# Optimization experiments

Hardware: AMD Instinct MI355X
Metric: run time of the kernel (lower is better)

## Reference

```python
import jax, jax.numpy as jnp
import numpy as np

DIM = 512
HEADS = 4
HEAD_DIM = DIM // HEADS
SCALE = HEAD_DIM ** -0.5


def _lin(x, W, b):
    # torch nn.Linear: y = x @ W.T + b, W is [out, in]
    return jnp.einsum('...i,oi->...o', x, W) + b


def setup_inputs() -> dict:
    key = jax.random.key(0)
    ks = jax.random.split(key, 20)
    f1 = jax.random.normal(ks[0], (4, 5, DIM, 10, 10), dtype=jnp.float32)
    f2 = jax.random.normal(ks[1], (4, 75, DIM, 10, 10), dtype=jnp.float32)
    names = ['k1', 'v1', 'q2', 'k2', 'v2', 'o1', 'o2']
    inp = {'f1': f1, 'f2': f2}
    for i, nm in enumerate(names):
        inp['W' + nm] = 0.02 * jax.random.normal(ks[2 + 2 * i], (DIM, DIM), dtype=jnp.float32)
        inp['b' + nm] = 0.02 * jax.random.normal(ks[3 + 2 * i], (DIM,), dtype=jnp.float32)
    return inp


def _forward(f1, f2, Wk1, bk1, Wv1, bv1, Wq2, bq2, Wk2, bk2, Wv2, bv2, Wo1, bo1, Wo2, bo2):
    B, n1, C, H, W = f1.shape
    n2 = f2.shape[1]
    L = H * W
    # [B,n,C,H,W] -> [B,n,L,C]
    f1t = f1.reshape(B, n1, C, L).transpose(0, 1, 3, 2)
    f2t = f2.reshape(B, n2, C, L).transpose(0, 1, 3, 2)

    def split_heads(x, n):  # [B,n,L,C] -> [B,heads,n*L,hd]
        return x.reshape(B, n * L, HEADS, HEAD_DIM).transpose(0, 2, 1, 3)

    def merge_heads(x, n):  # [B,heads,n*L,hd] -> [B,n,L,C]
        return x.transpose(0, 2, 1, 3).reshape(B, n, L, C)

    K1 = split_heads(_lin(f1t, Wk1, bk1), n1)
    V1 = split_heads(_lin(f1t, Wv1, bv1), n1)
    Q2 = split_heads(_lin(f2t, Wq2, bq2), n2)
    K2 = split_heads(_lin(f2t, Wk2, bk2), n2)  # computed as in original, unused downstream
    V2 = split_heads(_lin(f2t, Wv2, bv2), n2)

    # Query attends to support: [B,h,n2*L,n1*L]
    att_q = jax.nn.softmax(jnp.einsum('bhqd,bhkd->bhqk', Q2, K1) * SCALE, axis=-1)
    out2 = jnp.einsum('bhqk,bhkd->bhqd', att_q, V1)
    out2 = _lin(merge_heads(out2, n2), Wo2, bo2)
    out2 = out2.transpose(0, 1, 3, 2).reshape(B, n2, C, H, W)

    # Support attends to query: [B,h,n1*L,n2*L]
    att_s = jax.nn.softmax(jnp.einsum('bhsd,bhqd->bhsq', K1, Q2) * SCALE, axis=-1)
    out1 = jnp.einsum('bhsq,bhqd->bhsd', att_s, V2)
    out1 = _lin(merge_heads(out1, n1), Wo1, bo1)
    out1 = out1.transpose(0, 1, 3, 2).reshape(B, n1, C, H, W)
    return (out1, out2)


def reference(f1, f2, Wk1, bk1, Wv1, bv1, Wq2, bq2, Wk2, bk2, Wv2, bv2, Wo1, bo1, Wo2, bo2):
    return _forward(f1, f2, Wk1, bk1, Wv1, bv1, Wq2, bq2, Wk2, bk2, Wv2, bv2, Wo1, bo1, Wo2, bo2)
```

## Files before the change

kernel.cpp:

```cpp
#include <hip/hip_runtime.h>
#include <hip/hip_bf16.h>


#define QSCL  (0.08838834764831845f * 1.4426950408889634f)
#define KSPL  8
#define NRB2  59
#define NRB1  4

using bf16x8 = __attribute__((ext_vector_type(8))) short;
using f32x4  = __attribute__((ext_vector_type(4))) float;

__device__ inline ushort f2bf(float x) {
    union { float f; unsigned u; } v; v.f = x;
    unsigned r = v.u + 0x7fff + ((v.u >> 16) & 1);
    return (ushort)(r >> 16);
}

__device__ inline void gll16(const ushort* g, ushort* l) {
    __builtin_amdgcn_global_load_lds(
        (const __attribute__((address_space(1))) void*)g,
        (__attribute__((address_space(3))) void*)l, 16, 0, 0);
}

struct PreArgs { const float* w[6]; float s[6]; const float* f1; const float* f2; };

__global__ __launch_bounds__(256) void pre_kernel(
    PreArgs pa, ushort* __restrict__ Wb,
    ushort* __restrict__ f1t, ushort* __restrict__ f2t)
{
    __shared__ ushort Ts[100 * 136];
    const int t   = threadIdx.x;
    const int bid = blockIdx.x;

    if (bid < 1536) {
        const int wsel = bid >> 8;
        const float* src = pa.w[wsel];
        const float sc = pa.s[wsel];
        ushort* d = Wb + (size_t)wsel * 262144;
        const int idx = ((bid & 255) * 256 + t) * 4;
        const float4 v = *(const float4*)(src + idx);
        ushort4 o;
        o.x = f2bf(v.x * sc); o.y = f2bf(v.y * sc);
        o.z = f2bf(v.z * sc); o.w = f2bf(v.w * sc);
        *(ushort4*)(d + idx) = o;
        return;
    }

    const int bn = bid - 1536;
    const float* Xb;
    ushort* Yb;
    if (bn < 20) { Xb = pa.f1 + (size_t)bn * 51200;        Yb = f1t + (size_t)bn * 51200; }
    else         { Xb = pa.f2 + (size_t)(bn - 20) * 51200; Yb = f2t + (size_t)(bn - 20) * 51200; }

    for (int c0 = 0; c0 < 512; c0 += 128) {
        __syncthreads();
        #pragma unroll
        for (int i = 0; i < 50; ++i) {
            const int id = i * 256 + t;
            const int c = id / 100, l = id - c * 100;
            Ts[l * 136 + c] = f2bf(Xb[(size_t)(c0 + c) * 100 + l]);
        }
        __syncthreads();
        #pragma unroll
        for (int i = 0; i < 7; ++i) {
            const int id = i * 256 + t;
            if (id < 1600) {
                const int cg = id & 15, l = id >> 4;
                *(uint4*)(Yb + (size_t)l * 512 + c0 + cg * 8) =
                    *(const uint4*)&Ts[l * 136 + cg * 8];
            }
        }
    }
}

struct GemmJob {
    const ushort* A; const ushort* B;
    const float* bias; void* C;
    size_t sA, sB, sC;
    float bscale;
    int ldC, Mrows, Ncols, gx, gy, nblk;
};

template<int EPI, int BAXIS>
__global__ __launch_bounds__(256) void gemm_nt(GemmJob j0, GemmJob j1)
{
    __shared__ ushort smem[17408];
    ushort* As = smem;
    ushort* Bs = smem + 8192;

    const bool second = (int)blockIdx.x >= j0.nblk;
    const GemmJob& j = second ? j1 : j0;
    int id = blockIdx.x - (second ? j0.nblk : 0);

    const int bx = id % j.gx;
    const int rem = id / j.gx;
    const int by = rem % j.gy;
    const int bz = rem / j.gy;

    const int t    = threadIdx.x;
    const int lane = t & 63;
    const int w    = t >> 6;
    const int mw   = (w >> 1) * 64;
    const int nw   = (w & 1) * 64;
    const int m0   = bx * 128;
    const int n0   = by * 128;
    const int Mrows = j.Mrows, Ncols = j.Ncols, ldC = j.ldC;
    const ushort* Ab = j.A + (size_t)bz * j.sA;
    const ushort* Bb = j.B + (size_t)bz * j.sB;
    const float* bias = j.bias;

    f32x4 acc[4][4];
    #pragma unroll
    for (int i = 0; i < 4; ++i)
        #pragma unroll
        for (int jj = 0; jj < 4; ++jj) acc[i][jj] = (f32x4){0.f, 0.f, 0.f, 0.f};

    const int lr = lane >> 3;
    const int cb = lane & 7;

    for (int k0 = 0; k0 < 512; k0 += 64) {
        if (k0) __syncthreads();
        #pragma unroll
        for (int i = 0; i < 4; ++i) {
            const int row = w * 32 + i * 8 + lr;
            const int ar = min(m0 + row, Mrows - 1);
            gll16(Ab + (size_t)ar * 512 + k0 + ((cb ^ (row & 7)) * 8),
                  As + (w * 32 + i * 8) * 64);
            const int br = min(n0 + row, Ncols - 1);
            gll16(Bb + (size_t)br * 512 + k0 + ((cb ^ (row & 7)) * 8),
                  Bs + (w * 32 + i * 8) * 64);
        }
        __syncthreads();
        #pragma unroll
        for (int ks = 0; ks < 2; ++ks) {
            bf16x8 af[4], bv[4];
            #pragma unroll
            for (int mf = 0; mf < 4; ++mf) {
                const int row = mw + mf * 16 + (lane & 15);
                af[mf] = *(const bf16x8*)((const char*)As + row * 128 +
                          ((ks * 64 + (lane >> 4) * 16) ^ ((row & 7) << 4)));
            }
            #pragma unroll
            for (int nf = 0; nf < 4; ++nf) {
                const int row = nw + nf * 16 + (lane & 15);
                bv[nf] = *(const bf16x8*)((const char*)Bs + row * 128 +
                          ((ks * 64 + (lane >> 4) * 16) ^ ((row & 7) << 4)));
            }
            #pragma unroll
            for (int mf = 0; mf < 4; ++mf)
                #pragma unroll
                for (int nf = 0; nf < 4; ++nf)
                    acc[mf][nf] = __builtin_amdgcn_mfma_f32_16x16x32_bf16(
                        af[mf], bv[nf], acc[mf][nf], 0, 0, 0);
        }
    }
    __syncthreads();

    if (EPI == 0) {
        float bcol[4];
        if (BAXIS == 1) {
            #pragma unroll
            for (int nf = 0; nf < 4; ++nf)
                bcol[nf] = bias[n0 + nw + nf * 16 + (lane & 15)] * j.bscale;
        }
        ushort* Ts = smem;
        #pragma unroll
        for (int mf = 0; mf < 4; ++mf) {
            #pragma unroll
            for (int r = 0; r < 4; ++r) {
                const int row = mw + mf * 16 + (lane >> 4) * 4 + r;
                const float brow = (BAXIS == 0) ? bias[m0 + row] * j.bscale : 0.f;
                #pragma unroll
                for (int nf = 0; nf < 4; ++nf) {
                    const int col = nw + nf * 16 + (lane & 15);
                    const float v = acc[mf][nf][r] +
                                    ((BAXIS == 1) ? bcol[nf] : brow);
                    Ts[row * 136 + col] = f2bf(v);
                }
            }
        }
        __syncthreads();
        ushort* Cb = (ushort*)j.C + (size_t)bz * j.sC;
        #pragma unroll
        for (int i = 0; i < 8; ++i) {
            const int id2 = i * 256 + t;
            const int row = id2 >> 4, cg = id2 & 15;
            if (m0 + row < Mrows)
                *(uint4*)(Cb + (size_t)(m0 + row) * ldC + n0 + cg * 8) =
                    *(const uint4*)&Ts[row * 136 + cg * 8];
        }
    } else {
        float* Ts2 = (float*)smem;
        float* Cb = (float*)j.C + (size_t)bz * j.sC;
        const int colL = t & 127;
        const int rb2 = t >> 7;
        const int tg = n0 + colL;
        int nIdx = 0, lIdx = 0;
        if (tg < Ncols) { nIdx = tg / 100; lIdx = tg - nIdx * 100; }
        #pragma unroll
        for (int h = 0; h < 2; ++h) {
            __syncthreads();
            if ((mw >> 6) == h) {
                #pragma unroll
                for (int mf = 0; mf < 4; ++mf) {
                    #pragma unroll
                    for (int r = 0; r < 4; ++r) {
                        const int rowl = mf * 16 + (lane >> 4) * 4 + r;
                        const float brow = bias[m0 + h * 64 + rowl];
                        #pragma unroll
                        for (int nf = 0; nf < 4; ++nf) {
                            const int col = nw + nf * 16 + (lane & 15);
                            Ts2[rowl * 132 + col] = acc[mf][nf][r] + brow;
                        }
                    }
                }
            }
            __syncthreads();
            if (tg < Ncols) {
                float* dst = Cb + (size_t)nIdx * 51200 + lIdx;
                #pragma unroll
                for (int i = 0; i < 32; ++i) {
                    const int rowl = i * 2 + rb2;
                    const int c = m0 + h * 64 + rowl;
                    dst[(size_t)c * 100] = Ts2[rowl * 132 + colL];
                }
            }
        }
    }
}

__global__ __launch_bounds__(512, 4) void attn_mfma_kernel(
    const ushort* __restrict__ Q2, const ushort* __restrict__ K1,
    const ushort* __restrict__ V1t, const ushort* __restrict__ V2t,
    ushort* __restrict__ A2, float* __restrict__ PartO, float* __restrict__ Pml)
{
    __shared__ ushort Ks[64 * 128];
    __shared__ ushort Vs[128 * 64];

    const int t    = threadIdx.x;
    const int lane = t & 63;
    const int w    = t >> 6;

    const int flat = blockIdx.x;
    const int xcd = flat & 7, ii = flat >> 3;
    const bool dir2 = (ii >= 64);
    int rb, h, b, sp = 0;
    if (dir2) {
        const int w2 = xcd * 118 + (ii - 64);
        rb = w2 % NRB2;
        const int hb = w2 / NRB2;
        h = hb & 3; b = hb >> 2;
    } else {
        const int w1 = xcd * 64 + ii;
        rb = w1 & 3; sp = (w1 >> 2) & 7;
        const int hb = w1 >> 5;
        h = hb & 3; b = hb >> 2;
    }

    const int TR = dir2 ? 7500 : 500;
    const int TK = dir2 ? 500 : 7500;
    const int strideV = dir2 ? 512 : 7552;
    const ushort* R  = dir2 ? Q2 : K1;
    const ushort* Kt = dir2 ? K1 : Q2;
    const ushort* Vt = dir2 ? V1t : V2t;

    const int r0 = rb * 128;
    const int ho = h * 128;

    int kbeg = 0, kend = TK;
    if (!dir2) {
        kbeg = sp * 938;
        kend = kbeg + 938; if (kend > TK) kend = TK;
    }

    bf16x8 qa[4];
    {
        const ushort* Rb = R + (size_t)b * TR * 512;
        const int qrow = min(r0 + (w << 4) + (lane & 15), TR - 1);
        const ushort* qp = Rb + (size_t)qrow * 512 + ho + (lane >> 4) * 8;
        #pragma unroll
        for (int s = 0; s < 4; ++s)
            qa[s] = *(const bf16x8*)(qp + s * 32);
    }

    const ushort* Kb = Kt + (size_t)b * TK * 512;
    const ushort* Vb = Vt + ((size_t)b * 512 + ho) * strideV;

    const int krow_i = lane >> 4;
    const int kcol   = (lane & 15) * 8;
    const int vrow_i = lane >> 3;
    const int vcol   = (lane & 7) * 8;
    const int gq     = lane >> 4;

    float m_run = -3.0e38f, l_run = 0.f;
    f32x4 acc[8];
    #pragma unroll
    for (int g = 0; g < 8; ++g) acc[g] = (f32x4){0.f, 0.f, 0.f, 0.f};

    #pragma unroll
    for (int i = 0; i < 2; ++i) {
        const int kr = w * 8 + i * 4 + krow_i;
        gll16(Kb + (size_t)(kbeg + kr) * 512 + ho + (kcol ^ ((kr & 7) << 3)),
              Ks + (w * 8 + i * 4) * 128);
    }

    for (int kbase = kbeg; kbase < kend; kbase += 64) {
        #pragma unroll
        for (int i = 0; i < 2; ++i) {
            const int vd = w * 16 + i * 8 + vrow_i;
            gll16(Vb + (size_t)vd * strideV + kbase + (vcol ^ ((vd & 7) << 3)),
                  Vs + (w * 16 + i * 8) * 64);
        }
        asm volatile("s_waitcnt vmcnt(2)" ::: "memory");
        __builtin_amdgcn_s_barrier();
        __builtin_amdgcn_sched_barrier(0);

        f32x4 sf[4];
        __builtin_amdgcn_s_setprio(1);
        #pragma unroll
        for (int f = 0; f < 4; ++f) {
            f32x4 s = (f32x4){0.f, 0.f, 0.f, 0.f};
            const int kr = f * 16 + (lane & 15);
            const int kb2 = kr * 256, sw = (kr & 7) << 4, g16 = gq * 16;
            #pragma unroll
            for (int s4 = 0; s4 < 4; ++s4) {
                bf16x8 kf = *(const bf16x8*)((const char*)Ks + kb2 + ((s4 * 64 + g16) ^ sw));
                s = __builtin_amdgcn_mfma_f32_16x16x32_bf16(kf, qa[s4], s, 0, 0, 0);
            }
            sf[f] = s;
        }
        __builtin_amdgcn_s_setprio(0);

        if (kbase + 64 > kend) {
            #pragma unroll
            for (int f = 0; f < 4; ++f)
                #pragma unroll
                for (int r = 0; r < 4; ++r)
                    if (kbase + f * 16 + gq * 4 + r >= kend) sf[f][r] = -3.0e38f;
        }
        float mx = sf[0][0];
        #pragma unroll
        for (int f = 0; f < 4; ++f)
            #pragma unroll
            for (int r = 0; r < 4; ++r) mx = fmaxf(mx, sf[f][r]);
        mx = fmaxf(mx, __shfl_xor(mx, 16));
        mx = fmaxf(mx, __shfl_xor(mx, 32));
        if (__any(mx > m_run + 11.0f)) {
            const float mn = fmaxf(m_run, mx);
            const float sc = __builtin_amdgcn_exp2f(m_run - mn);
            m_run = mn;
            l_run *= sc;
            float scal4[4];
            #pragma unroll
            for (int r = 0; r < 4; ++r)
                scal4[r] = __shfl(sc, (lane & 48) + gq * 4 + r);
            #pragma unroll
            for (int g = 0; g < 8; ++g)
                #pragma unroll
                for (int r = 0; r < 4; ++r) acc[g][r] *= scal4[r];
        }
        float rs = 0.f;
        #pragma unroll
        for (int f = 0; f < 4; ++f)
            #pragma unroll
            for (int r = 0; r < 4; ++r) {
                const float p = __builtin_amdgcn_exp2f(sf[f][r] - m_run);
                sf[f][r] = p;
                rs += p;
            }
        rs += __shfl_xor(rs, 16);
        rs += __shfl_xor(rs, 32);
        l_run += rs;

        uint pk[4][2];
        #pragma unroll
        for (int f = 0; f < 4; ++f) {
            const float x0 = sf[f][0], x1 = sf[f][1], x2 = sf[f][2], x3 = sf[f][3];
            asm("v_cvt_pk_bf16_f32 %0, %1, %2" : "=v"(pk[f][0]) : "v"(x0), "v"(x1));
            asm("v_cvt_pk_bf16_f32 %0, %1, %2" : "=v"(pk[f][1]) : "v"(x2), "v"(x3));
        }
        union { uint u[4]; bf16x8 v; } pa0, pa1;
        #pragma unroll
        for (int u = 0; u < 4; ++u) {
            const int srcl = (lane & 15) + ((lane & 16) << 1) + ((u >> 1) << 4);
            const uint a0 = (uint)__shfl((int)pk[0][u & 1], srcl);
            const uint b0 = (uint)__shfl((int)pk[1][u & 1], srcl);
            const uint a1 = (uint)__shfl((int)pk[2][u & 1], srcl);
            const uint b1 = (uint)__shfl((int)pk[3][u & 1], srcl);
            pa0.u[u] = (lane & 32) ? b0 : a0;
            pa1.u[u] = (lane & 32) ? b1 : a1;
        }

        asm volatile("s_waitcnt vmcnt(0)" ::: "memory");
        __builtin_amdgcn_s_barrier();
        __builtin_amdgcn_sched_barrier(0);

        if (kbase + 64 < kend) {
            #pragma unroll
            for (int i = 0; i < 2; ++i) {
                const int kr = w * 8 + i * 4 + krow_i;
                gll16(Kb + (size_t)(kbase + 64 + kr) * 512 + ho + (kcol ^ ((kr & 7) << 3)),
                      Ks + (w * 8 + i * 4) * 128);
            }
        }

        {
            const int g16 = gq * 16;
            __builtin_amdgcn_s_setprio(1);
            #pragma unroll
            for (int g = 0; g < 8; ++g) {
                const int dr = g * 16 + (lane & 15);
                const int vb = dr * 128, vsw = (dr & 7) << 4;
                bf16x8 v0 = *(const bf16x8*)((const char*)Vs + vb + ((g16) ^ vsw));
                bf16x8 v1 = *(const bf16x8*)((const char*)Vs + vb + ((64 + g16) ^ vsw));
                acc[g] = __builtin_amdgcn_mfma_f32_16x16x32_bf16(pa0.v, v0, acc[g], 0, 0, 0);
                acc[g] = __builtin_amdgcn_mfma_f32_16x16x32_bf16(pa1.v, v1, acc[g], 0, 0, 0);
            }
            __builtin_amdgcn_s_setprio(0);
        }
        __builtin_amdgcn_s_barrier();
        __builtin_amdgcn_sched_barrier(0);
    }

    const int rloc = (w << 4) + (gq << 2);
    if (dir2) {
        float linv[4];
        #pragma unroll
        for (int r = 0; r < 4; ++r)
            linv[r] = 1.f / __shfl(l_run, (lane & 48) + gq * 4 + r);
        #pragma unroll
        for (int r = 0; r < 4; ++r) {
            const int row = r0 + rloc + r;
            if (row < TR) {
                ushort* Ab2 = A2 + ((size_t)b * TR + row) * 512 + ho + (lane & 15);
                #pragma unroll
                for (int g = 0; g < 8; ++g) Ab2[g * 16] = f2bf(acc[g][r] * linv[r]);
            }
        }
    } else {
        const size_t tile = (((size_t)b * 4 + h) * NRB1 + rb) * KSPL + sp;
        float* Po = PartO + tile * (128 * 128);
        float* Pm = Pml + tile * 256;
        #pragma unroll
        for (int r = 0; r < 4; ++r) {
            const int row = rloc + r;
            float* pp = Po + row * 128 + (lane & 15);
            #pragma unroll
            for (int g = 0; g < 8; ++g) pp[g * 16] = acc[g][r];
        }
        if (lane < 16) {
            Pm[(w << 4) + lane] = m_run;
            Pm[128 + (w << 4) + lane] = l_run;
        }
    }
}

__global__ __launch_bounds__(256) void attn_combine_kernel(
    const float* __restrict__ PartO, const float* __restrict__ Pml,
    ushort* __restrict__ Aout, int TR)
{
    const int t = threadIdx.x;
    const int rb = blockIdx.x >> 1, half = blockIdx.x & 1;
    const int h = blockIdx.y, b = blockIdx.z;
    const int row = half * 64 + (t >> 2);
    const int dq = (t & 3) * 32;
    const int r0 = rb * 128;
    const size_t tbase = (((size_t)b * 4 + h) * NRB1 + rb) * KSPL;

    float M = -3.0e38f;
    #pragma unroll
    for (int i = 0; i < KSPL; ++i)
        M = fmaxf(M, Pml[(tbase + i) * 256 + row]);
    float wt[KSPL], L = 0.f;
    #pragma unroll
    for (int i = 0; i < KSPL; ++i) {
        const float wi = __builtin_amdgcn_exp2f(Pml[(tbase + i) * 256 + row] - M);
        wt[i] = wi;
        L += wi * Pml[(tbase + i) * 256 + 128 + row];
    }
    if (r0 + row >= TR) return;
    const float invL = 1.f / L;

    float o[32];
    #pragma unroll
    for (int j = 0; j < 32; ++j) o[j] = 0.f;
    #pragma unroll
    for (int i = 0; i < KSPL; ++i) {
        const float* pp = PartO + (tbase + i) * (128 * 128) + row * 128 + dq;
        #pragma unroll
        for (int j = 0; j < 32; j += 4) {
            const float4 v = *(const float4*)(pp + j);
            o[j] += wt[i] * v.x; o[j+1] += wt[i] * v.y;
            o[j+2] += wt[i] * v.z; o[j+3] += wt[i] * v.w;
        }
    }
    ushort* Ab = Aout + ((size_t)b * TR + r0 + row) * 512 + h * 128 + dq;
    #pragma unroll
    for (int j = 0; j < 32; j += 4) {
        ushort4 v;
        v.x = f2bf(o[j] * invL); v.y = f2bf(o[j+1] * invL);
        v.z = f2bf(o[j+2] * invL); v.w = f2bf(o[j+3] * invL);
        *(ushort4*)(Ab + j) = v;
    }
}

extern "C" void kernel_launch(void* const* d_in, const int* in_sizes, int n_in,
                              void* d_out, int out_size, void* d_ws, size_t ws_size,
                              hipStream_t stream) {
    const float* f1  = (const float*)d_in[0];
    const float* f2  = (const float*)d_in[1];
    const float* Wk1 = (const float*)d_in[2];
    const float* bk1 = (const float*)d_in[3];
    const float* Wv1 = (const float*)d_in[4];
    const float* bv1 = (const float*)d_in[5];
    const float* Wq2 = (const float*)d_in[6];
    const float* bq2 = (const float*)d_in[7];
    const float* Wv2 = (const float*)d_in[10];
    const float* bv2 = (const float*)d_in[11];
    const float* Wo1 = (const float*)d_in[12];
    const float* bo1 = (const float*)d_in[13];
    const float* Wo2 = (const float*)d_in[14];
    const float* bo2 = (const float*)d_in[15];
    float* out = (float*)d_out;

    ushort* f1t = (ushort*)d_ws;
    ushort* f2t = f1t + (size_t)1024000;
    ushort* Wb  = f2t + (size_t)15360000;
    ushort* K1  = Wb  + (size_t)1572864;
    ushort* Q2  = K1  + (size_t)1024000;
    ushort* V1t = Q2  + (size_t)15360000;
    ushort* V2t = V1t + (size_t)1048576;
    ushort* A1  = V2t + (size_t)15466496;
    ushort* A2  = A1  + (size_t)1024000;
    float* PartO = (float*)(A2 + (size_t)15360000);
    float* Pml   = PartO + (size_t)512*128*128;

    const dim3 blk(256);

    const ushort* Wk1b = Wb;
    const ushort* Wv1b = Wb + 262144;
    const ushort* Wq2b = Wb + 2*262144;
    const ushort* Wv2b = Wb + 3*262144;
    const ushort* Wo1b = Wb + 4*262144;
    const ushort* Wo2b = Wb + 5*262144;

    PreArgs pa;
    pa.w[0]=Wk1; pa.w[1]=Wv1; pa.w[2]=Wq2; pa.w[3]=Wv2; pa.w[4]=Wo1; pa.w[5]=Wo2;
    pa.s[0]=1.f; pa.s[1]=1.f; pa.s[2]=QSCL; pa.s[3]=1.f; pa.s[4]=1.f; pa.s[5]=1.f;
    pa.f1 = f1; pa.f2 = f2;
    pre_kernel<<<dim3(1856), blk, 0, stream>>>(pa, Wb, f1t, f2t);

    GemmJob jK{f1t, Wk1b, bk1, K1, 0, 0, 0, 1.f, 512, 2000, 512, 16, 4, 64};
    GemmJob jQ{f2t, Wq2b, bq2, Q2, 0, 0, 0, QSCL, 512, 30000, 512, 235, 4, 940};
    gemm_nt<0,1><<<dim3(1004), blk, 0, stream>>>(jK, jQ);

    GemmJob jV1{Wv1b, f1t, bv1, V1t, 0, (size_t)500*512, (size_t)512*512, 1.f,
                512, 512, 500, 4, 4, 64};
    GemmJob jV2{Wv2b, f2t, bv2, V2t, 0, (size_t)7500*512, (size_t)512*7552, 1.f,
                7552, 512, 7500, 4, 59, 944};
    gemm_nt<0,0><<<dim3(1008), blk, 0, stream>>>(jV1, jV2);

    attn_mfma_kernel<<<dim3(1456), dim3(512), 0, stream>>>(
        Q2, K1, V1t, V2t, A2, PartO, Pml);
    attn_combine_kernel<<<dim3(8, 4, 4), blk, 0, stream>>>(PartO, Pml, A1, 500);

    GemmJob jO1{Wo1b, A1, bo1, out, 0, (size_t)500*512, (size_t)5*51200, 1.f,
                0, 512, 500, 4, 4, 64};
    GemmJob jO2{Wo2b, A2, bo2, out + (size_t)1024000, 0, (size_t)7500*512,
                (size_t)75*51200, 1.f, 0, 512, 7500, 4, 59, 944};
    gemm_nt<2,0><<<dim3(1008), blk, 0, stream>>>(jO1, jO2);
}
```

Baseline: 258.6 us.

## Merge QK and V projection GEMMs into one launch with XCD-aware block remap

The K1/Q2 projection and V1/V2 projection GEMM launches are fused into a single launch covering four jobs. Block ids are remapped so that each of the 8 XCDs gets a contiguous range of work, and the K/Q jobs iterate the N dimension fastest, so neighbouring tiles that share A rows land on the same XCD's L2. This aims to remove one launch gap and tail, and to improve L2 reuse. The bias axis becomes a runtime field, which adds per-thread branching in the epilogue.

```diff
diff --git a/kernel.cpp b/kernel.cpp
--- a/kernel.cpp
+++ b/kernel.cpp
@@ -78,32 +78,47 @@
     const float* bias; void* C;
     size_t sA, sB, sC;
     float bscale;
-    int ldC, Mrows, Ncols, gx, gy, nblk;
+    int ldC, Mrows, Ncols, gx, gy, fastn, baxis, nblk;
 };
 
-template<int EPI, int BAXIS>
-__global__ __launch_bounds__(256) void gemm_nt(GemmJob j0, GemmJob j1)
+struct GemmJobs { GemmJob j0, j1, j2, j3; int ntot; };
+
+template<int EPI>
+__global__ __launch_bounds__(256) void gemm_nt(GemmJobs J)
 {
     __shared__ ushort smem[17408];
     ushort* As = smem;
     ushort* Bs = smem + 8192;
 
-    const bool second = (int)blockIdx.x >= j0.nblk;
-    const GemmJob& j = second ? j1 : j0;
-    int id = blockIdx.x - (second ? j0.nblk : 0);
-
-    const int bx = id % j.gx;
+    const int ntot = J.ntot;
+    const int q8 = ntot >> 3, r8 = ntot & 7;
+    const int xcd = blockIdx.x & 7, ii = blockIdx.x >> 3;
+    const int work = (xcd < r8 ? xcd * (q8 + 1)
+                               : r8 * (q8 + 1) + (xcd - r8) * q8) + ii;
+
+    GemmJob j; int id;
+    {
+        const int c0 = J.j0.nblk;
+        const int c1 = c0 + J.j1.nblk;
+        const int c2 = c1 + J.j2.nblk;
+        if (work < c0)      { j = J.j0; id = work; }
+        else if (work < c1) { j = J.j1; id = work - c0; }
+        else if (work < c2) { j = J.j2; id = work - c1; }
+        else                { j = J.j3; id = work - c2; }
+    }
+
+    const int fx = id % j.gx;
     const int rem = id / j.gx;
-    const int by = rem % j.gy;
+    const int fy = rem % j.gy;
     const int bz = rem / j.gy;
+    const int m0 = (j.fastn ? fy : fx) * 128;
+    const int n0 = (j.fastn ? fx : fy) * 128;
 
     const int t    = threadIdx.x;
     const int lane = t & 63;
     const int w    = t >> 6;
     const int mw   = (w >> 1) * 64;
     const int nw   = (w & 1) * 64;
-    const int m0   = bx * 128;
-    const int n0   = by * 128;
     const int Mrows = j.Mrows, Ncols = j.Ncols, ldC = j.ldC;
     const ushort* Ab = j.A + (size_t)bz * j.sA;
     const ushort* Bb = j.B + (size_t)bz * j.sB;
@@ -158,7 +173,7 @@
 
     if (EPI == 0) {
         float bcol[4];
-        if (BAXIS == 1) {
+        if (j.baxis == 1) {
             #pragma unroll
             for (int nf = 0; nf < 4; ++nf)
                 bcol[nf] = bias[n0 + nw + nf * 16 + (lane & 15)] * j.bscale;
@@ -169,12 +184,12 @@
             #pragma unroll
             for (int r = 0; r < 4; ++r) {
                 const int row = mw + mf * 16 + (lane >> 4) * 4 + r;
-                const float brow = (BAXIS == 0) ? bias[m0 + row] * j.bscale : 0.f;
+                const float brow = (j.baxis == 0) ? bias[m0 + row] * j.bscale : 0.f;
                 #pragma unroll
                 for (int nf = 0; nf < 4; ++nf) {
                     const int col = nw + nf * 16 + (lane & 15);
                     const float v = acc[mf][nf][r] +
-                                    ((BAXIS == 1) ? bcol[nf] : brow);
+                                    ((j.baxis == 1) ? bcol[nf] : brow);
                     Ts[row * 136 + col] = f2bf(v);
                 }
             }
@@ -550,23 +565,26 @@
     pa.f1 = f1; pa.f2 = f2;
     pre_kernel<<<dim3(1856), blk, 0, stream>>>(pa, Wb, f1t, f2t);
 
-    GemmJob jK{f1t, Wk1b, bk1, K1, 0, 0, 0, 1.f, 512, 2000, 512, 16, 4, 64};
-    GemmJob jQ{f2t, Wq2b, bq2, Q2, 0, 0, 0, QSCL, 512, 30000, 512, 235, 4, 940};
-    gemm_nt<0,1><<<dim3(1004), blk, 0, stream>>>(jK, jQ);
-
+    GemmJob jK {f1t, Wk1b, bk1, K1, 0, 0, 0, 1.f, 512, 2000, 512,
+                4, 16, 1, 1, 64};
+    GemmJob jQ {f2t, Wq2b, bq2, Q2, 0, 0, 0, QSCL, 512, 30000, 512,
+                4, 235, 1, 1, 940};
     GemmJob jV1{Wv1b, f1t, bv1, V1t, 0, (size_t)500*512, (size_t)512*512, 1.f,
-                512, 512, 500, 4, 4, 64};
+                512, 512, 500, 4, 4, 0, 0, 64};
     GemmJob jV2{Wv2b, f2t, bv2, V2t, 0, (size_t)7500*512, (size_t)512*7552, 1.f,
-                7552, 512, 7500, 4, 59, 944};
-    gemm_nt<0,0><<<dim3(1008), blk, 0, stream>>>(jV1, jV2);
+                7552, 512, 7500, 4, 59, 0, 0, 944};
+    GemmJobs JP{jK, jQ, jV1, jV2, 2012};
+    gemm_nt<0><<<dim3(2012), blk, 0, stream>>>(JP);
 
     attn_mfma_kernel<<<dim3(1456), dim3(512), 0, stream>>>(
         Q2, K1, V1t, V2t, A2, PartO, Pml);
     attn_combine_kernel<<<dim3(8, 4, 4), blk, 0, stream>>>(PartO, Pml, A1, 500);
 
     GemmJob jO1{Wo1b, A1, bo1, out, 0, (size_t)500*512, (size_t)5*51200, 1.f,
-                0, 512, 500, 4, 4, 64};
+                0, 512, 500, 4, 4, 0, 0, 64};
     GemmJob jO2{Wo2b, A2, bo2, out + (size_t)1024000, 0, (size_t)7500*512,
-                (size_t)75*51200, 1.f, 0, 512, 7500, 4, 59, 944};
-    gemm_nt<2,0><<<dim3(1008), blk, 0, stream>>>(jO1, jO2);
-}
+                (size_t)75*51200, 1.f, 0, 512, 7500, 4, 59, 0, 0, 944};
+    GemmJob jZ{};
+    GemmJobs JO{jO1, jO2, jZ, jZ, 1008};
+    gemm_nt<2><<<dim3(1008), blk, 0, stream>>>(JO);
+}
```

Result: faster. 238.1 us (-7.9%).
